# Kernel optimization log

Hardware: AMD Instinct MI355X
Metric: run time of the kernel (lower is better)

## Reference

```python
import jax, jax.numpy as jnp
import numpy as np

M = 16       # learned queries
K = 64       # top-k sparse tokens
HEADS = 4    # attention heads
LN_EPS = 1e-5


def _l2norm(x, eps=1e-12):
    n = jnp.linalg.norm(x, axis=-1, keepdims=True)
    return x / jnp.maximum(n, eps)


def _layernorm(x, w, b):
    mu = x.mean(-1, keepdims=True)
    var = x.var(-1, keepdims=True)
    return (x - mu) * jax.lax.rsqrt(var + LN_EPS) * w + b


def setup_inputs() -> dict:
    key = jax.random.key(0)
    ks = jax.random.split(key, 12)
    B, N, C, T, TD, D = 4, 16384, 1024, 20, 512, 64
    s = lambda k, sh: jax.random.normal(k, sh, jnp.float32) * 0.02
    return {
        "image_features": jax.random.normal(ks[0], (B, N, C), jnp.float32),
        "text_features": jax.random.normal(ks[1], (B, T, TD), jnp.float32),
        "Wd": s(ks[2], (C, D)), "bd": jnp.zeros((D,), jnp.float32),
        "Wu": s(ks[3], (D, C)), "bu": jnp.zeros((C,), jnp.float32),
        "m_queries": jax.random.normal(ks[4], (1, M, D), jnp.float32),
        "Wq": s(ks[5], (D, D)), "bq": jnp.zeros((D,), jnp.float32),
        "Wk": s(ks[6], (D, D)), "bk": jnp.zeros((D,), jnp.float32),
        "Wv": s(ks[7], (D, D)), "bv": jnp.zeros((D,), jnp.float32),
        "Wo": s(ks[8], (D, D)), "bo": jnp.zeros((D,), jnp.float32),
        "ln_w": jnp.ones((D,), jnp.float32), "ln_b": jnp.zeros((D,), jnp.float32),
        "gamma": jnp.float32(0.1),
    }


def reference(image_features, text_features, Wd, bd, Wu, bu, m_queries,
              Wq, bq, Wk, bk, Wv, bv, Wo, bo, ln_w, ln_b, gamma):
    B, N, C = image_features.shape
    D = Wd.shape[1]
    identity = image_features

    # down-project + exact GELU (dropout is identity at eval)
    a = jax.nn.gelu(image_features @ Wd + bd, approximate=False)  # [B,N,D]

    # tokens_of_interest=None, text_consistency_loss=False:
    # slice text to projected dim, take token 0 as key
    sel = text_features[:, 0, :D]                                  # [B,D]
    scores = jnp.einsum("bnd,bd->bn", _l2norm(a), _l2norm(sel))    # [B,N]

    # top-k mask -> nonzero gives row-sorted indices per batch
    _, idx = jax.lax.top_k(scores, K)                              # [B,K]
    idx = jnp.sort(idx, axis=1)

    sparse = jnp.take_along_axis(a, idx[:, :, None], axis=1)       # [B,K,D]
    queries = jnp.broadcast_to(m_queries, (B, M, D))
    comb = jnp.concatenate([queries, sparse], axis=1)              # [B,M+K,D]

    x = _layernorm(comb, ln_w, ln_b)
    H, Dh = HEADS, D // HEADS
    S = M + K
    q = (x @ Wq + bq).reshape(B, S, H, Dh)
    k = (x @ Wk + bk).reshape(B, S, H, Dh)
    v = (x @ Wv + bv).reshape(B, S, H, Dh)
    att = jnp.einsum("bshd,bthd->bhst", q, k) / jnp.sqrt(jnp.float32(Dh))
    att = jax.nn.softmax(att, axis=-1)
    o = jnp.einsum("bhst,bthd->bshd", att, v).reshape(B, S, D)
    attn_out = o @ Wo + bo

    enh = comb + attn_out
    enh_sparse = enh[:, M:, :]                                     # [B,K,D]

    # scatter enhanced sparse tokens back into full sequence
    brow = jnp.arange(B)[:, None]
    delta_proj = jnp.zeros_like(a).at[brow, idx].set(enh_sparse)   # [B,N,D]
    delta_x = delta_proj @ Wu + bu                                 # [B,N,C]

    return identity + delta_x * gamma
```

## Files before the change

kernel.cpp:

```cpp
#include <hip/hip_runtime.h>
#include <hip/hip_bf16.h>
#include <math.h>

typedef __bf16 bf16x8 __attribute__((ext_vector_type(8)));
typedef unsigned short u16x8 __attribute__((ext_vector_type(8)));
typedef float f32x4 __attribute__((ext_vector_type(4)));

#define CDIM 1024
#define DDIM 64
#define NB   16384
#define NROWS 65536

__device__ __forceinline__ unsigned short f2bf(float x){
  unsigned int u = __float_as_uint(x);
  unsigned int lsb = (u >> 16) & 1u;
  u += 0x7fffu + lsb;
  return (unsigned short)(u >> 16);
}

__global__ __launch_bounds__(256) void dsa_prep(
    const float* __restrict__ Wd, const float* __restrict__ tf,
    unsigned short* __restrict__ Wf, float* __restrict__ seln){
  int bb = blockIdx.x, tid = threadIdx.x;
  if (bb < 32){
    int g = bb*256 + tid;
    int lane = g & 63, tj = g >> 6;
    int n  = ((tj & 3) << 4) + (lane & 15);
    int k0 = ((tj >> 2) << 5) + ((lane >> 4) << 3);
    u16x8 uv;
    #pragma unroll
    for (int e=0;e<8;e++) uv[e] = f2bf(Wd[(k0+e)*DDIM + n]);
    *(u16x8*)(Wf + (size_t)g*8) = uv;
  } else {
    int w = tid >> 6, lane = tid & 63;
    float x = tf[w*(20*512) + lane];
    float sq = x*x;
    #pragma unroll
    for (int m=1; m<64; m<<=1) sq += __shfl_xor(sq, m);
    seln[w*64 + lane] = x / fmaxf(sqrtf(sq), 1e-12f);
  }
}

__global__ __launch_bounds__(256) void dsa_main(
    const float* __restrict__ X, const unsigned short* __restrict__ Wf,
    const float* __restrict__ bd, const float* __restrict__ bu,
    const float* __restrict__ gam, const float* __restrict__ seln,
    float* __restrict__ out, float* __restrict__ a_out, float* __restrict__ scores)
{
  const int tid  = threadIdx.x;
  const int lane = tid & 63, w = tid >> 6;
  const int row0 = blockIdx.x*64 + w*16;
  const int batch = blockIdx.x >> 8;
  const float gamma = gam[0];
  const int lr = lane & 15, lq = lane >> 4;

  const size_t rowoff = (size_t)(row0 + lr)*CDIM + lq*8;
  const float* xp = X   + rowoff;
  float*       op = out + rowoff;
  const float* bup = bu + lq*8;
  const bf16x8* wf8 = (const bf16x8*)Wf;

  f32x4 acc[4] = {};

  #pragma unroll 2
  for (int t = 0; t < 32; ++t){
    f32x4 xa = *(const f32x4*)(xp + t*32);
    f32x4 xb = *(const f32x4*)(xp + t*32 + 4);
    bf16x8 bv0 = wf8[(t*4+0)*64 + lane];
    bf16x8 bv1 = wf8[(t*4+1)*64 + lane];
    bf16x8 bv2 = wf8[(t*4+2)*64 + lane];
    bf16x8 bv3 = wf8[(t*4+3)*64 + lane];
    f32x4 ba = *(const f32x4*)(bup + t*32);
    f32x4 bb = *(const f32x4*)(bup + t*32 + 4);
    f32x4 oa = xa + gamma*ba;
    f32x4 ob = xb + gamma*bb;
    __builtin_nontemporal_store(oa, (f32x4*)(op + t*32));
    __builtin_nontemporal_store(ob, (f32x4*)(op + t*32 + 4));
    union { u16x8 u; bf16x8 b; } cv;
    cv.u[0]=f2bf(xa[0]); cv.u[1]=f2bf(xa[1]); cv.u[2]=f2bf(xa[2]); cv.u[3]=f2bf(xa[3]);
    cv.u[4]=f2bf(xb[0]); cv.u[5]=f2bf(xb[1]); cv.u[6]=f2bf(xb[2]); cv.u[7]=f2bf(xb[3]);
    acc[0] = __builtin_amdgcn_mfma_f32_16x16x32_bf16(cv.b, bv0, acc[0], 0,0,0);
    acc[1] = __builtin_amdgcn_mfma_f32_16x16x32_bf16(cv.b, bv1, acc[1], 0,0,0);
    acc[2] = __builtin_amdgcn_mfma_f32_16x16x32_bf16(cv.b, bv2, acc[2], 0,0,0);
    acc[3] = __builtin_amdgcn_mfma_f32_16x16x32_bf16(cv.b, bv3, acc[3], 0,0,0);
  }

  const float* selb = seln + batch*64;
  float ss[4] = {0,0,0,0}, dt[4] = {0,0,0,0};
  float gv[4][4];
  #pragma unroll
  for (int j=0;j<4;j++){
    int col = 16*j + lr;
    float bdc = bd[col];
    float sc  = selb[col];
    #pragma unroll
    for (int r=0;r<4;r++){
      float y = acc[j][r] + bdc;
      float g = 0.5f * y * (1.0f + erff(y * 0.70710678118654752f));
      gv[j][r] = g;
      ss[r] += g*g;
      dt[r] += g*sc;
    }
  }
  #pragma unroll
  for (int r=0;r<4;r++){
    int row = row0 + 4*lq + r;
    #pragma unroll
    for (int j=0;j<4;j++)
      a_out[(size_t)row*DDIM + 16*j + lr] = gv[j][r];
  }
  #pragma unroll
  for (int m=1;m<16;m<<=1){
    #pragma unroll
    for (int r=0;r<4;r++){
      ss[r] += __shfl_xor(ss[r], m);
      dt[r] += __shfl_xor(dt[r], m);
    }
  }
  if (lr == 0){
    #pragma unroll
    for (int r=0;r<4;r++)
      scores[row0 + 4*lq + r] = dt[r] / fmaxf(sqrtf(ss[r]), 1e-12f);
  }
}

__global__ __launch_bounds__(1024) void dsa_topk(const float* __restrict__ scores,
                                                 int* __restrict__ idxo){
  const int b = blockIdx.x, tid = threadIdx.x;
  const float* s = scores + b*NB;
  const int base = tid*16;
  unsigned key[16];
  #pragma unroll
  for (int i=0;i<16;i+=4){
    f32x4 f = *(const f32x4*)(s + base + i);
    #pragma unroll
    for (int c=0;c<4;c++){
      unsigned u = __float_as_uint(f[c]);
      key[i+c] = (u & 0x80000000u) ? ~u : (u | 0x80000000u);
    }
  }

  __shared__ unsigned bins[256];
  __shared__ unsigned sh_pref, sh_R;
  __shared__ int selIdx[64];
  __shared__ int eqIdx[256];
  __shared__ unsigned selCnt, eqCnt;

  unsigned prefix = 0, R = 64;
  for (int pass=0; pass<4; ++pass){
    const int shift = 24 - pass*8;
    if (tid < 256) bins[tid] = 0;
    __syncthreads();
    #pragma unroll
    for (int i=0;i<16;i++){
      unsigned k = key[i];
      bool ok;
      if (pass == 0) ok = true;
      else           ok = ((k >> (shift+8)) == prefix);
      if (ok) atomicAdd(&bins[(k >> shift) & 255u], 1u);
    }
    __syncthreads();
    if (tid < 64){
      unsigned c0 = bins[tid*4+0], c1 = bins[tid*4+1];
      unsigned c2 = bins[tid*4+2], c3 = bins[tid*4+3];
      unsigned gs = c0+c1+c2+c3;
      unsigned suf = gs;
      #pragma unroll
      for (int m=1;m<64;m<<=1){
        unsigned o = __shfl_down(suf, m);
        if (tid + m < 64) suf += o;
      }
      unsigned above = suf - gs;
      if (above < R && R <= suf){
        unsigned a3 = above;
        unsigned a2 = a3 + c3;
        unsigned a1 = a2 + c2;
        unsigned a0 = a1 + c1;
        unsigned bb, ab;
        if      (R <= a3 + c3){ bb = 3; ab = a3; }
        else if (R <= a2 + c2){ bb = 2; ab = a2; }
        else if (R <= a1 + c1){ bb = 1; ab = a1; }
        else                  { bb = 0; ab = a0; }
        sh_pref = (prefix << 8) | (tid*4 + bb);
        sh_R = R - ab;
      }
    }
    __syncthreads();
    prefix = sh_pref; R = sh_R;
    __syncthreads();
  }
  if (tid == 0){ selCnt = 0; eqCnt = 0; }
  __syncthreads();
  #pragma unroll
  for (int i=0;i<16;i++){
    unsigned k = key[i];
    if (k > prefix){
      selIdx[atomicAdd(&selCnt, 1u)] = base + i;
    } else if (k == prefix){
      unsigned p = atomicAdd(&eqCnt, 1u);
      if (p < 256) eqIdx[p] = base + i;
    }
  }
  __syncthreads();
  if (tid == 0){
    unsigned n = eqCnt < 256u ? eqCnt : 256u;
    unsigned have = selCnt;
    for (unsigned r2 = 0; r2 < R; ++r2){
      int best = 0x7fffffff, bi = -1;
      for (unsigned e=0; e<n; e++)
        if (eqIdx[e] < best){ best = eqIdx[e]; bi = (int)e; }
      selIdx[have + r2] = best;
      eqIdx[bi] = 0x7fffffff;
    }
  }
  __syncthreads();
  if (tid < 64){
    int x = selIdx[tid];
    #pragma unroll
    for (int size=2; size<=64; size<<=1){
      #pragma unroll
      for (int stride=size>>1; stride>0; stride>>=1){
        int ox = __shfl_xor(x, stride);
        bool up = ((tid & size) == 0);
        bool takeMin = (((tid & stride) == 0) == up);
        int mn = x < ox ? x : ox, mx = x < ox ? ox : x;
        x = takeMin ? mn : mx;
      }
    }
    idxo[b*64 + tid] = x;
  }
}

__global__ __launch_bounds__(512) void dsa_tail(
    const float* __restrict__ a, const float* __restrict__ mq, const int* __restrict__ idx,
    const float* __restrict__ lnw, const float* __restrict__ lnb,
    const float* __restrict__ Wq, const float* __restrict__ bq,
    const float* __restrict__ Wk, const float* __restrict__ bk,
    const float* __restrict__ Wv, const float* __restrict__ bv,
    const float* __restrict__ Wo, const float* __restrict__ bo,
    float* __restrict__ enh)
{
  __shared__ float xln[80][64];
  __shared__ float qS[80][64];
  __shared__ float vS[80][68];
  __shared__ float kT[64][81];
  __shared__ float oS[80][64];
  __shared__ float WoS[64][64];
  __shared__ float rowbuf[8][84];
  __shared__ int   sidx[64];

  const int b = blockIdx.x, tid = threadIdx.x;
  const int w = tid >> 6, lane = tid & 63;

  if (tid < 64) sidx[tid] = idx[b*64 + tid];
  for (int e = tid; e < 4096; e += 512) WoS[e>>6][e&63] = Wo[e];
  __syncthreads();

  {
    float lw = lnw[lane], lb = lnb[lane];
    float vals[10];
    #pragma unroll
    for (int i=0;i<10;i++){
      int s = w + 8*i;
      vals[i] = (s < 16) ? mq[s*64 + lane]
                         : a[((size_t)b*NB + sidx[s-16])*64 + lane];
    }
    #pragma unroll
    for (int i=0;i<10;i++){
      int s = w + 8*i;
      float val = vals[i];
      float sm = val, sq = val*val;
      #pragma unroll
      for (int m=1;m<64;m<<=1){ sm += __shfl_xor(sm,m); sq += __shfl_xor(sq,m); }
      float mu  = sm * (1.0f/64.0f);
      float var = sq * (1.0f/64.0f) - mu*mu;
      xln[s][lane] = (val - mu) * rsqrtf(var + 1e-5f) * lw + lb;
    }
  }
  __syncthreads();

  #pragma unroll 1
  for (int m = 0; m < 3; ++m){
    const float* Wm = (m==0) ? Wq : (m==1) ? Wk : Wv;
    const float* bm = (m==0) ? bq : (m==1) ? bk : bv;
    float wreg[64];
    #pragma unroll
    for (int c=0;c<64;c++) wreg[c] = Wm[c*64 + lane];
    float bias = bm[lane];
    #pragma unroll 1
    for (int s = w; s < 80; s += 8){
      float accv = bias;
      #pragma unroll
      for (int c4=0;c4<16;c4++){
        f32x4 x4 = *(const f32x4*)&xln[s][c4*4];
        accv += x4[0]*wreg[c4*4+0] + x4[1]*wreg[c4*4+1]
              + x4[2]*wreg[c4*4+2] + x4[3]*wreg[c4*4+3];
      }
      if (m==0)      qS[s][lane]  = accv;
      else if (m==1) kT[lane][s]  = accv;
      else           vS[s][lane]  = accv;
    }
  }
  __syncthreads();

  {
    const int h = w >> 1, h16 = h*16;
    const int i0 = 16 + (w & 1)*32;
    const int jj = lane >> 4, dd = lane & 15;
    #pragma unroll 2
    for (int ii = 0; ii < 32; ++ii){
      int i = i0 + ii;
      float v0 = 0.f, v1 = 0.f;
      #pragma unroll
      for (int d=0; d<16; ++d){
        float qd = qS[i][h16+d];
        v0 = fmaf(qd, kT[h16+d][lane],    v0);
        v1 = fmaf(qd, kT[h16+d][64 + dd], v1);
      }
      v0 *= 0.25f; v1 *= 0.25f;
      float mx = fmaxf(v0, v1);
      #pragma unroll
      for (int m2=1;m2<64;m2<<=1) mx = fmaxf(mx, __shfl_xor(mx,m2));
      float e0 = expf(v0 - mx);
      float e1 = expf(v1 - mx);
      float sm = e0 + ((lane < 16) ? e1 : 0.f);
      #pragma unroll
      for (int m2=1;m2<64;m2<<=1) sm += __shfl_xor(sm,m2);
      float inv = 1.0f / sm;
      rowbuf[w][lane] = e0 * inv;
      if (lane < 16) rowbuf[w][64+dd] = e1 * inv;
      float part = 0.f;
      #pragma unroll
      for (int tt=0; tt<20; ++tt){
        int j = jj*20 + tt;
        part = fmaf(rowbuf[w][j], vS[j][h16+dd], part);
      }
      part += __shfl_xor(part, 16);
      part += __shfl_xor(part, 32);
      if (lane < 16) oS[i][h16+dd] = part;
    }
  }
  __syncthreads();

  for (int e = tid; e < 4096; e += 512){
    int s16 = e >> 6, cc = e & 63;
    float accv = bo[cc];
    #pragma unroll
    for (int d4=0; d4<16; ++d4){
      f32x4 o4 = *(const f32x4*)&oS[16+s16][d4*4];
      accv += o4[0]*WoS[d4*4+0][cc] + o4[1]*WoS[d4*4+1][cc]
            + o4[2]*WoS[d4*4+2][cc] + o4[3]*WoS[d4*4+3][cc];
    }
    float cmb = a[((size_t)b*NB + sidx[s16])*64 + cc];
    enh[(b*64 + s16)*64 + cc] = cmb + accv;
  }
}

__global__ __launch_bounds__(256) void dsa_scatter(
    const float* __restrict__ enh, const float* __restrict__ Wu,
    const float* __restrict__ gam, const int* __restrict__ idx,
    float* __restrict__ out)
{
  int blk = blockIdx.x;
  int b = blk >> 6, j = blk & 63;
  int tid = threadIdx.x;
  __shared__ float er[64];
  if (tid < 64) er[tid] = enh[(b*64+j)*64 + tid];
  __syncthreads();
  int n = idx[b*64 + j];
  float gamma = gam[0];
  int c0 = tid*4;
  float ax=0.f, ay=0.f, az=0.f, aw=0.f;
  #pragma unroll 8
  for (int d=0; d<64; ++d){
    float ev = er[d];
    f32x4 wr = *(const f32x4*)(Wu + d*CDIM + c0);
    ax += ev*wr[0]; ay += ev*wr[1]; az += ev*wr[2]; aw += ev*wr[3];
  }
  float* op = out + ((size_t)b*NB + n)*CDIM + c0;
  f32x4 cu = *(f32x4*)op;
  cu[0] += gamma*ax; cu[1] += gamma*ay; cu[2] += gamma*az; cu[3] += gamma*aw;
  *(f32x4*)op = cu;
}

extern "C" void kernel_launch(void* const* d_in, const int* in_sizes, int n_in,
                              void* d_out, int out_size, void* d_ws, size_t ws_size,
                              hipStream_t stream) {
  const float* X    = (const float*)d_in[0];
  const float* tf   = (const float*)d_in[1];
  const float* Wd   = (const float*)d_in[2];
  const float* bd   = (const float*)d_in[3];
  const float* Wu   = (const float*)d_in[4];
  const float* bu   = (const float*)d_in[5];
  const float* mq   = (const float*)d_in[6];
  const float* Wq   = (const float*)d_in[7];
  const float* bq   = (const float*)d_in[8];
  const float* Wk   = (const float*)d_in[9];
  const float* bk   = (const float*)d_in[10];
  const float* Wv   = (const float*)d_in[11];
  const float* bv   = (const float*)d_in[12];
  const float* Wo   = (const float*)d_in[13];
  const float* bo   = (const float*)d_in[14];
  const float* lnw  = (const float*)d_in[15];
  const float* lnb  = (const float*)d_in[16];
  const float* gam  = (const float*)d_in[17];
  float* out = (float*)d_out;

  float* ws_a               = (float*)d_ws;
  unsigned short* ws_wf     = (unsigned short*)(ws_a + (size_t)NROWS*DDIM);
  float* ws_scores          = (float*)(ws_wf + 64*CDIM);
  float* ws_seln            = ws_scores + NROWS;
  int*   ws_idx             = (int*)(ws_seln + 256);
  float* ws_enh             = (float*)(ws_idx + 256);

  dsa_prep   <<<33,   256, 0, stream>>>(Wd, tf, ws_wf, ws_seln);
  dsa_main   <<<1024, 256, 0, stream>>>(X, ws_wf, bd, bu, gam, ws_seln,
                                        out, ws_a, ws_scores);
  dsa_topk   <<<4,   1024, 0, stream>>>(ws_scores, ws_idx);
  dsa_tail   <<<4,    512, 0, stream>>>(ws_a, mq, ws_idx, lnw, lnb,
                                        Wq, bq, Wk, bk, Wv, bv, Wo, bo, ws_enh);
  dsa_scatter<<<256,  256, 0, stream>>>(ws_enh, Wu, gam, ws_idx, out);
}
```

Baseline: 229.2 us.

## Stage Wd tiles in double-buffered LDS and software-pipeline X loads in main GEMM

The main down-projection kernel now copies the bf16 weight panel into a double-buffered shared-memory tile once per block instead of having every wave read it from global memory. It also prefetches the next chunk of X rows into registers while computing the current one. The gamma*bu bias is precomputed in the prep kernel and kept in LDS. Other changes: hardware bf16 conversion replaces the manual rounding, and the output stores are no longer nontemporal. The costs are more register pressure and LDS use (about 36 KB per block), plus block-wide syncs that may lower occupancy on this memory-bound streaming kernel.

```diff
diff --git a/kernel.cpp b/kernel.cpp
--- a/kernel.cpp
+++ b/kernel.cpp
@@ -20,7 +20,9 @@
 
 __global__ __launch_bounds__(256) void dsa_prep(
     const float* __restrict__ Wd, const float* __restrict__ tf,
-    unsigned short* __restrict__ Wf, float* __restrict__ seln){
+    const float* __restrict__ bu, const float* __restrict__ gam,
+    unsigned short* __restrict__ Wf, float* __restrict__ seln,
+    float* __restrict__ gbu){
   int bb = blockIdx.x, tid = threadIdx.x;
   if (bb < 32){
     int g = bb*256 + tid;
@@ -38,52 +40,91 @@
     #pragma unroll
     for (int m=1; m<64; m<<=1) sq += __shfl_xor(sq, m);
     seln[w*64 + lane] = x / fmaxf(sqrtf(sq), 1e-12f);
+    float g = gam[0];
+    f32x4 b4 = *(const f32x4*)(bu + tid*4);
+    *(f32x4*)(gbu + tid*4) = g*b4;
   }
 }
 
 __global__ __launch_bounds__(256) void dsa_main(
     const float* __restrict__ X, const unsigned short* __restrict__ Wf,
-    const float* __restrict__ bd, const float* __restrict__ bu,
-    const float* __restrict__ gam, const float* __restrict__ seln,
+    const float* __restrict__ bd, const float* __restrict__ gbu,
+    const float* __restrict__ seln,
     float* __restrict__ out, float* __restrict__ a_out, float* __restrict__ scores)
 {
+  __shared__ __align__(16) unsigned short Bs[2][8192];
+  __shared__ __align__(16) float gbS[1024];
   const int tid  = threadIdx.x;
   const int lane = tid & 63, w = tid >> 6;
+  const int lr = lane & 15, lq = lane >> 4;
   const int row0 = blockIdx.x*64 + w*16;
   const int batch = blockIdx.x >> 8;
-  const float gamma = gam[0];
-  const int lr = lane & 15, lq = lane >> 4;
 
   const size_t rowoff = (size_t)(row0 + lr)*CDIM + lq*8;
   const float* xp = X   + rowoff;
   float*       op = out + rowoff;
-  const float* bup = bu + lq*8;
-  const bf16x8* wf8 = (const bf16x8*)Wf;
-
+
+  f32x4 xr0[4][2], xr1[4][2];
+  uint4 st[4];
   f32x4 acc[4] = {};
 
-  #pragma unroll 2
-  for (int t = 0; t < 32; ++t){
-    f32x4 xa = *(const f32x4*)(xp + t*32);
-    f32x4 xb = *(const f32x4*)(xp + t*32 + 4);
-    bf16x8 bv0 = wf8[(t*4+0)*64 + lane];
-    bf16x8 bv1 = wf8[(t*4+1)*64 + lane];
-    bf16x8 bv2 = wf8[(t*4+2)*64 + lane];
-    bf16x8 bv3 = wf8[(t*4+3)*64 + lane];
-    f32x4 ba = *(const f32x4*)(bup + t*32);
-    f32x4 bb = *(const f32x4*)(bup + t*32 + 4);
-    f32x4 oa = xa + gamma*ba;
-    f32x4 ob = xb + gamma*bb;
-    __builtin_nontemporal_store(oa, (f32x4*)(op + t*32));
-    __builtin_nontemporal_store(ob, (f32x4*)(op + t*32 + 4));
-    union { u16x8 u; bf16x8 b; } cv;
-    cv.u[0]=f2bf(xa[0]); cv.u[1]=f2bf(xa[1]); cv.u[2]=f2bf(xa[2]); cv.u[3]=f2bf(xa[3]);
-    cv.u[4]=f2bf(xb[0]); cv.u[5]=f2bf(xb[1]); cv.u[6]=f2bf(xb[2]); cv.u[7]=f2bf(xb[3]);
-    acc[0] = __builtin_amdgcn_mfma_f32_16x16x32_bf16(cv.b, bv0, acc[0], 0,0,0);
-    acc[1] = __builtin_amdgcn_mfma_f32_16x16x32_bf16(cv.b, bv1, acc[1], 0,0,0);
-    acc[2] = __builtin_amdgcn_mfma_f32_16x16x32_bf16(cv.b, bv2, acc[2], 0,0,0);
-    acc[3] = __builtin_amdgcn_mfma_f32_16x16x32_bf16(cv.b, bv3, acc[3], 0,0,0);
-  }
+#define LD_B(P) { \
+    st[0] = *(const uint4*)(Wf + (P)*8192 + 0*2048 + tid*8); \
+    st[1] = *(const uint4*)(Wf + (P)*8192 + 1*2048 + tid*8); \
+    st[2] = *(const uint4*)(Wf + (P)*8192 + 2*2048 + tid*8); \
+    st[3] = *(const uint4*)(Wf + (P)*8192 + 3*2048 + tid*8); }
+#define ST_B(BUFI) { \
+    *(uint4*)(&Bs[BUFI][0*2048 + tid*8]) = st[0]; \
+    *(uint4*)(&Bs[BUFI][1*2048 + tid*8]) = st[1]; \
+    *(uint4*)(&Bs[BUFI][2*2048 + tid*8]) = st[2]; \
+    *(uint4*)(&Bs[BUFI][3*2048 + tid*8]) = st[3]; }
+#define LD_A(R, P) { \
+    R[0][0]=*(const f32x4*)(xp+(P)*128+  0); R[0][1]=*(const f32x4*)(xp+(P)*128+  4); \
+    R[1][0]=*(const f32x4*)(xp+(P)*128+ 32); R[1][1]=*(const f32x4*)(xp+(P)*128+ 36); \
+    R[2][0]=*(const f32x4*)(xp+(P)*128+ 64); R[2][1]=*(const f32x4*)(xp+(P)*128+ 68); \
+    R[3][0]=*(const f32x4*)(xp+(P)*128+ 96); R[3][1]=*(const f32x4*)(xp+(P)*128+100); }
+#define STEP(BUFI, TL, R, P) { \
+    f32x4 xa = R[TL][0], xb = R[TL][1]; \
+    f32x4 g0 = *(const f32x4*)(&gbS[(P)*128 + (TL)*32 + lq*8]); \
+    f32x4 g1 = *(const f32x4*)(&gbS[(P)*128 + (TL)*32 + lq*8 + 4]); \
+    *(f32x4*)(op + (P)*128 + (TL)*32)     = xa + g0; \
+    *(f32x4*)(op + (P)*128 + (TL)*32 + 4) = xb + g1; \
+    bf16x8 av; \
+    av[0]=(__bf16)xa[0]; av[1]=(__bf16)xa[1]; av[2]=(__bf16)xa[2]; av[3]=(__bf16)xa[3]; \
+    av[4]=(__bf16)xb[0]; av[5]=(__bf16)xb[1]; av[6]=(__bf16)xb[2]; av[7]=(__bf16)xb[3]; \
+    bf16x8 b0 = *(const bf16x8*)(&Bs[BUFI][(TL)*2048 + 0*512 + lane*8]); \
+    bf16x8 b1 = *(const bf16x8*)(&Bs[BUFI][(TL)*2048 + 1*512 + lane*8]); \
+    bf16x8 b2 = *(const bf16x8*)(&Bs[BUFI][(TL)*2048 + 2*512 + lane*8]); \
+    bf16x8 b3 = *(const bf16x8*)(&Bs[BUFI][(TL)*2048 + 3*512 + lane*8]); \
+    acc[0] = __builtin_amdgcn_mfma_f32_16x16x32_bf16(av, b0, acc[0], 0,0,0); \
+    acc[1] = __builtin_amdgcn_mfma_f32_16x16x32_bf16(av, b1, acc[1], 0,0,0); \
+    acc[2] = __builtin_amdgcn_mfma_f32_16x16x32_bf16(av, b2, acc[2], 0,0,0); \
+    acc[3] = __builtin_amdgcn_mfma_f32_16x16x32_bf16(av, b3, acc[3], 0,0,0); }
+#define PHASE(K, RCUR, RNXT) { \
+    LD_B((K)+1); LD_A(RNXT, (K)+1); \
+    STEP((K)&1, 0, RCUR, K) STEP((K)&1, 1, RCUR, K) \
+    STEP((K)&1, 2, RCUR, K) STEP((K)&1, 3, RCUR, K) \
+    ST_B(((K)+1)&1); __syncthreads(); }
+
+  { f32x4 t = *(const f32x4*)(gbu + tid*4); *(f32x4*)(&gbS[tid*4]) = t; }
+  LD_B(0); LD_A(xr0, 0);
+  ST_B(0);
+  __syncthreads();
+
+  PHASE(0, xr0, xr1)
+  PHASE(1, xr1, xr0)
+  PHASE(2, xr0, xr1)
+  PHASE(3, xr1, xr0)
+  PHASE(4, xr0, xr1)
+  PHASE(5, xr1, xr0)
+  PHASE(6, xr0, xr1)
+  STEP(1, 0, xr1, 7) STEP(1, 1, xr1, 7) STEP(1, 2, xr1, 7) STEP(1, 3, xr1, 7)
+
+#undef LD_B
+#undef ST_B
+#undef LD_A
+#undef STEP
+#undef PHASE
 
   const float* selb = seln + batch*64;
   float ss[4] = {0,0,0,0}, dt[4] = {0,0,0,0};
@@ -410,11 +451,12 @@
   unsigned short* ws_wf     = (unsigned short*)(ws_a + (size_t)NROWS*DDIM);
   float* ws_scores          = (float*)(ws_wf + 64*CDIM);
   float* ws_seln            = ws_scores + NROWS;
-  int*   ws_idx             = (int*)(ws_seln + 256);
+  float* ws_gbu             = ws_seln + 256;
+  int*   ws_idx             = (int*)(ws_gbu + 1024);
   float* ws_enh             = (float*)(ws_idx + 256);
 
-  dsa_prep   <<<33,   256, 0, stream>>>(Wd, tf, ws_wf, ws_seln);
-  dsa_main   <<<1024, 256, 0, stream>>>(X, ws_wf, bd, bu, gam, ws_seln,
+  dsa_prep   <<<33,   256, 0, stream>>>(Wd, tf, bu, gam, ws_wf, ws_seln, ws_gbu);
+  dsa_main   <<<1024, 256, 0, stream>>>(X, ws_wf, bd, ws_gbu, ws_seln,
                                         out, ws_a, ws_scores);
   dsa_topk   <<<4,   1024, 0, stream>>>(ws_scores, ws_idx);
   dsa_tail   <<<4,    512, 0, stream>>>(ws_a, mq, ws_idx, lnw, lnb,
```

After: 211.7 us. -7.6%, faster.

## Double-buffer X tiles into LDS via async global_load_lds in main GEMM

Applied to the files above, without the earlier changes.

The main down-projection kernel now streams each wave's 16x1024 slice of X into a swizzled, double-buffered LDS region using direct global-to-LDS loads. This overlaps the next chunk's fetch with the current chunk's MFMA and output writes. gamma*bu is precomputed once in the prep kernel and staged in LDS, and the output stores become ordinary stores instead of nontemporal ones. The bf16 conversion now uses a native cast rather than manual rounding. The manual vmcnt waits make correctness depend on counting outstanding loads exactly, and the 36KB of LDS per block limits occupancy.

```diff
diff --git a/kernel.cpp b/kernel.cpp
--- a/kernel.cpp
+++ b/kernel.cpp
@@ -18,9 +18,17 @@
   return (unsigned short)(u >> 16);
 }
 
+__device__ __forceinline__ void load_lds16(const float* g, float* l){
+  __builtin_amdgcn_global_load_lds(
+      (const __attribute__((address_space(1))) void*)g,
+      (__attribute__((address_space(3))) void*)l, 16, 0, 0);
+}
+
 __global__ __launch_bounds__(256) void dsa_prep(
     const float* __restrict__ Wd, const float* __restrict__ tf,
-    unsigned short* __restrict__ Wf, float* __restrict__ seln){
+    const float* __restrict__ bu, const float* __restrict__ gam,
+    unsigned short* __restrict__ Wf, float* __restrict__ seln,
+    float* __restrict__ gbu){
   int bb = blockIdx.x, tid = threadIdx.x;
   if (bb < 32){
     int g = bb*256 + tid;
@@ -38,52 +46,94 @@
     #pragma unroll
     for (int m=1; m<64; m<<=1) sq += __shfl_xor(sq, m);
     seln[w*64 + lane] = x / fmaxf(sqrtf(sq), 1e-12f);
-  }
-}
-
-__global__ __launch_bounds__(256) void dsa_main(
+    float g = gam[0];
+    f32x4 b4 = *(const f32x4*)(bu + tid*4);
+    *(f32x4*)(gbu + tid*4) = g*b4;
+  }
+}
+
+__global__ __launch_bounds__(256, 4) void dsa_main(
     const float* __restrict__ X, const unsigned short* __restrict__ Wf,
-    const float* __restrict__ bd, const float* __restrict__ bu,
-    const float* __restrict__ gam, const float* __restrict__ seln,
+    const float* __restrict__ bd, const float* __restrict__ gbu,
+    const float* __restrict__ seln,
     float* __restrict__ out, float* __restrict__ a_out, float* __restrict__ scores)
 {
+  __shared__ __align__(16) float AsF[8192];
+  __shared__ __align__(16) float gbS[1024];
   const int tid  = threadIdx.x;
   const int lane = tid & 63, w = tid >> 6;
+  const int lr = lane & 15, lq = lane >> 4;
   const int row0 = blockIdx.x*64 + w*16;
   const int batch = blockIdx.x >> 8;
-  const float gamma = gam[0];
-  const int lr = lane & 15, lq = lane >> 4;
-
-  const size_t rowoff = (size_t)(row0 + lr)*CDIM + lq*8;
-  const float* xp = X   + rowoff;
-  float*       op = out + rowoff;
-  const float* bup = bu + lq*8;
+
+  { f32x4 t = *(const f32x4*)(gbu + tid*4); *(f32x4*)(gbS + tid*4) = t; }
+  __syncthreads();
+
+  const int rsub = lane >> 4;
+  const int ch   = lane & 15;
+  const float* gbase = X + (size_t)(row0 + rsub)*CDIM;
+  float* asw = AsF + w*2048;
+  float* op  = out + (size_t)(row0 + lr)*CDIM;
   const bf16x8* wf8 = (const bf16x8*)Wf;
 
+  bf16x8 B[8];
   f32x4 acc[4] = {};
 
-  #pragma unroll 2
-  for (int t = 0; t < 32; ++t){
-    f32x4 xa = *(const f32x4*)(xp + t*32);
-    f32x4 xb = *(const f32x4*)(xp + t*32 + 4);
-    bf16x8 bv0 = wf8[(t*4+0)*64 + lane];
-    bf16x8 bv1 = wf8[(t*4+1)*64 + lane];
-    bf16x8 bv2 = wf8[(t*4+2)*64 + lane];
-    bf16x8 bv3 = wf8[(t*4+3)*64 + lane];
-    f32x4 ba = *(const f32x4*)(bup + t*32);
-    f32x4 bb = *(const f32x4*)(bup + t*32 + 4);
-    f32x4 oa = xa + gamma*ba;
-    f32x4 ob = xb + gamma*bb;
-    __builtin_nontemporal_store(oa, (f32x4*)(op + t*32));
-    __builtin_nontemporal_store(ob, (f32x4*)(op + t*32 + 4));
-    union { u16x8 u; bf16x8 b; } cv;
-    cv.u[0]=f2bf(xa[0]); cv.u[1]=f2bf(xa[1]); cv.u[2]=f2bf(xa[2]); cv.u[3]=f2bf(xa[3]);
-    cv.u[4]=f2bf(xb[0]); cv.u[5]=f2bf(xb[1]); cv.u[6]=f2bf(xb[2]); cv.u[7]=f2bf(xb[3]);
-    acc[0] = __builtin_amdgcn_mfma_f32_16x16x32_bf16(cv.b, bv0, acc[0], 0,0,0);
-    acc[1] = __builtin_amdgcn_mfma_f32_16x16x32_bf16(cv.b, bv1, acc[1], 0,0,0);
-    acc[2] = __builtin_amdgcn_mfma_f32_16x16x32_bf16(cv.b, bv2, acc[2], 0,0,0);
-    acc[3] = __builtin_amdgcn_mfma_f32_16x16x32_bf16(cv.b, bv3, acc[3], 0,0,0);
-  }
+#define DMA(P, SL) { \
+    { int gc = ch ^ ((0*4 + rsub)&7); \
+      load_lds16(gbase + (size_t)(0*4)*CDIM + (P)*64 + gc*4, asw + (SL)*1024 + 0*256); } \
+    { int gc = ch ^ ((1*4 + rsub)&7); \
+      load_lds16(gbase + (size_t)(1*4)*CDIM + (P)*64 + gc*4, asw + (SL)*1024 + 1*256); } \
+    { int gc = ch ^ ((2*4 + rsub)&7); \
+      load_lds16(gbase + (size_t)(2*4)*CDIM + (P)*64 + gc*4, asw + (SL)*1024 + 2*256); } \
+    { int gc = ch ^ ((3*4 + rsub)&7); \
+      load_lds16(gbase + (size_t)(3*4)*CDIM + (P)*64 + gc*4, asw + (SL)*1024 + 3*256); } }
+
+#define LDB(P) { \
+    B[0] = wf8[(((P)*2+0)*4+0)*64 + lane]; \
+    B[1] = wf8[(((P)*2+0)*4+1)*64 + lane]; \
+    B[2] = wf8[(((P)*2+0)*4+2)*64 + lane]; \
+    B[3] = wf8[(((P)*2+0)*4+3)*64 + lane]; \
+    B[4] = wf8[(((P)*2+1)*4+0)*64 + lane]; \
+    B[5] = wf8[(((P)*2+1)*4+1)*64 + lane]; \
+    B[6] = wf8[(((P)*2+1)*4+2)*64 + lane]; \
+    B[7] = wf8[(((P)*2+1)*4+3)*64 + lane]; }
+
+#define STEP(P, S, SL) { \
+    int c0 = (((S)*8 + lq*2 + 0) ^ (lr & 7)); \
+    int c1 = (((S)*8 + lq*2 + 1) ^ (lr & 7)); \
+    f32x4 xa = *(const f32x4*)(asw + (SL)*1024 + lr*64 + c0*4); \
+    f32x4 xb = *(const f32x4*)(asw + (SL)*1024 + lr*64 + c1*4); \
+    f32x4 g0 = *(const f32x4*)(gbS + (P)*64 + (S)*32 + lq*8); \
+    f32x4 g1 = *(const f32x4*)(gbS + (P)*64 + (S)*32 + lq*8 + 4); \
+    *(f32x4*)(op + (P)*64 + (S)*32 + lq*8)     = xa + g0; \
+    *(f32x4*)(op + (P)*64 + (S)*32 + lq*8 + 4) = xb + g1; \
+    bf16x8 av; \
+    av[0]=(__bf16)xa[0]; av[1]=(__bf16)xa[1]; av[2]=(__bf16)xa[2]; av[3]=(__bf16)xa[3]; \
+    av[4]=(__bf16)xb[0]; av[5]=(__bf16)xb[1]; av[6]=(__bf16)xb[2]; av[7]=(__bf16)xb[3]; \
+    acc[0] = __builtin_amdgcn_mfma_f32_16x16x32_bf16(av, B[4*(S)+0], acc[0], 0,0,0); \
+    acc[1] = __builtin_amdgcn_mfma_f32_16x16x32_bf16(av, B[4*(S)+1], acc[1], 0,0,0); \
+    acc[2] = __builtin_amdgcn_mfma_f32_16x16x32_bf16(av, B[4*(S)+2], acc[2], 0,0,0); \
+    acc[3] = __builtin_amdgcn_mfma_f32_16x16x32_bf16(av, B[4*(S)+3], acc[3], 0,0,0); }
+
+#define PH(P) { \
+    DMA((P)+1, ((P)+1)&1) \
+    LDB(P) \
+    asm volatile("s_waitcnt vmcnt(12)" ::: "memory"); \
+    STEP(P, 0, (P)&1) STEP(P, 1, (P)&1) \
+    asm volatile("" ::: "memory"); }
+
+  DMA(0, 0)
+  PH(0)  PH(1)  PH(2)  PH(3)  PH(4)  PH(5)  PH(6)  PH(7)
+  PH(8)  PH(9)  PH(10) PH(11) PH(12) PH(13) PH(14)
+  LDB(15)
+  asm volatile("s_waitcnt vmcnt(8)" ::: "memory");
+  STEP(15, 0, 1) STEP(15, 1, 1)
+
+#undef DMA
+#undef LDB
+#undef STEP
+#undef PH
 
   const float* selb = seln + batch*64;
   float ss[4] = {0,0,0,0}, dt[4] = {0,0,0,0};
@@ -410,11 +460,12 @@
   unsigned short* ws_wf     = (unsigned short*)(ws_a + (size_t)NROWS*DDIM);
   float* ws_scores          = (float*)(ws_wf + 64*CDIM);
   float* ws_seln            = ws_scores + NROWS;
-  int*   ws_idx             = (int*)(ws_seln + 256);
+  float* ws_gbu             = ws_seln + 256;
+  int*   ws_idx             = (int*)(ws_gbu + 1024);
   float* ws_enh             = (float*)(ws_idx + 256);
 
-  dsa_prep   <<<33,   256, 0, stream>>>(Wd, tf, ws_wf, ws_seln);
-  dsa_main   <<<1024, 256, 0, stream>>>(X, ws_wf, bd, bu, gam, ws_seln,
+  dsa_prep   <<<33,   256, 0, stream>>>(Wd, tf, bu, gam, ws_wf, ws_seln, ws_gbu);
+  dsa_main   <<<1024, 256, 0, stream>>>(X, ws_wf, bd, ws_gbu, ws_seln,
                                         out, ws_a, ws_scores);
   dsa_topk   <<<4,   1024, 0, stream>>>(ws_scores, ws_idx);
   dsa_tail   <<<4,    512, 0, stream>>>(ws_a, mq, ws_idx, lnw, lnb,
```

Result: faster. 220.8 us (-3.7%).

## Software-pipeline X and weight loads in main GEMM loop and precompute gamma*bu

Applied to the files above, without the earlier changes.

The main streaming loop now prefetches X tiles and bf16 weight fragments two iterations ahead using a triple-buffered register ring, and the loop is fully unrolled. gamma*bu is precomputed in the prep kernel and staged into shared memory, so the loop no longer reads bu from global memory or multiplies by gamma. Output stores become regular stores instead of nontemporal stores, and the float-to-bf16 conversion switches from a manual rounding routine to the native cast. The aim is to hide global memory latency in a bandwidth-bound loop, at the cost of more register pressure, which may reduce occupancy.

```diff
diff --git a/kernel.cpp b/kernel.cpp
--- a/kernel.cpp
+++ b/kernel.cpp
@@ -20,7 +20,9 @@
 
 __global__ __launch_bounds__(256) void dsa_prep(
     const float* __restrict__ Wd, const float* __restrict__ tf,
-    unsigned short* __restrict__ Wf, float* __restrict__ seln){
+    const float* __restrict__ bu, const float* __restrict__ gam,
+    unsigned short* __restrict__ Wf, float* __restrict__ seln,
+    float* __restrict__ gbu){
   int bb = blockIdx.x, tid = threadIdx.x;
   if (bb < 32){
     int g = bb*256 + tid;
@@ -38,52 +40,63 @@
     #pragma unroll
     for (int m=1; m<64; m<<=1) sq += __shfl_xor(sq, m);
     seln[w*64 + lane] = x / fmaxf(sqrtf(sq), 1e-12f);
+    float g = gam[0];
+    f32x4 b4 = *(const f32x4*)(bu + tid*4);
+    *(f32x4*)(gbu + tid*4) = g*b4;
   }
 }
 
 __global__ __launch_bounds__(256) void dsa_main(
     const float* __restrict__ X, const unsigned short* __restrict__ Wf,
-    const float* __restrict__ bd, const float* __restrict__ bu,
-    const float* __restrict__ gam, const float* __restrict__ seln,
+    const float* __restrict__ bd, const float* __restrict__ gbu,
+    const float* __restrict__ seln,
     float* __restrict__ out, float* __restrict__ a_out, float* __restrict__ scores)
 {
+  __shared__ __align__(16) float gbS[1024];
   const int tid  = threadIdx.x;
   const int lane = tid & 63, w = tid >> 6;
+  const int lr = lane & 15, lq = lane >> 4;
   const int row0 = blockIdx.x*64 + w*16;
   const int batch = blockIdx.x >> 8;
-  const float gamma = gam[0];
-  const int lr = lane & 15, lq = lane >> 4;
-
-  const size_t rowoff = (size_t)(row0 + lr)*CDIM + lq*8;
-  const float* xp = X   + rowoff;
-  float*       op = out + rowoff;
-  const float* bup = bu + lq*8;
+
+  { f32x4 t = *(const f32x4*)(gbu + tid*4); *(f32x4*)(gbS + tid*4) = t; }
+  __syncthreads();
+
+  const float* xp = X   + (size_t)(row0 + lr)*CDIM + lq*8;
+  float*       op = out + (size_t)(row0 + lr)*CDIM + lq*8;
   const bf16x8* wf8 = (const bf16x8*)Wf;
 
-  f32x4 acc[4] = {};
-
-  #pragma unroll 2
+  f32x4  xa[3], xb[3];
+  bf16x8 B[3][4];
+  f32x4  acc[4] = {};
+
+#define LDX(T) { xa[(T)%3] = *(const f32x4*)(xp + (T)*32); \
+                 xb[(T)%3] = *(const f32x4*)(xp + (T)*32 + 4); }
+#define LDBF(T) { B[(T)%3][0] = wf8[((T)*4+0)*64 + lane]; \
+                  B[(T)%3][1] = wf8[((T)*4+1)*64 + lane]; \
+                  B[(T)%3][2] = wf8[((T)*4+2)*64 + lane]; \
+                  B[(T)%3][3] = wf8[((T)*4+3)*64 + lane]; }
+
+  LDX(0) LDBF(0)
+  LDX(1) LDBF(1)
+  #pragma unroll
   for (int t = 0; t < 32; ++t){
-    f32x4 xa = *(const f32x4*)(xp + t*32);
-    f32x4 xb = *(const f32x4*)(xp + t*32 + 4);
-    bf16x8 bv0 = wf8[(t*4+0)*64 + lane];
-    bf16x8 bv1 = wf8[(t*4+1)*64 + lane];
-    bf16x8 bv2 = wf8[(t*4+2)*64 + lane];
-    bf16x8 bv3 = wf8[(t*4+3)*64 + lane];
-    f32x4 ba = *(const f32x4*)(bup + t*32);
-    f32x4 bb = *(const f32x4*)(bup + t*32 + 4);
-    f32x4 oa = xa + gamma*ba;
-    f32x4 ob = xb + gamma*bb;
-    __builtin_nontemporal_store(oa, (f32x4*)(op + t*32));
-    __builtin_nontemporal_store(ob, (f32x4*)(op + t*32 + 4));
-    union { u16x8 u; bf16x8 b; } cv;
-    cv.u[0]=f2bf(xa[0]); cv.u[1]=f2bf(xa[1]); cv.u[2]=f2bf(xa[2]); cv.u[3]=f2bf(xa[3]);
-    cv.u[4]=f2bf(xb[0]); cv.u[5]=f2bf(xb[1]); cv.u[6]=f2bf(xb[2]); cv.u[7]=f2bf(xb[3]);
-    acc[0] = __builtin_amdgcn_mfma_f32_16x16x32_bf16(cv.b, bv0, acc[0], 0,0,0);
-    acc[1] = __builtin_amdgcn_mfma_f32_16x16x32_bf16(cv.b, bv1, acc[1], 0,0,0);
-    acc[2] = __builtin_amdgcn_mfma_f32_16x16x32_bf16(cv.b, bv2, acc[2], 0,0,0);
-    acc[3] = __builtin_amdgcn_mfma_f32_16x16x32_bf16(cv.b, bv3, acc[3], 0,0,0);
-  }
+    if (t + 2 < 32){ LDX(t+2) LDBF(t+2) }
+    f32x4 g0 = *(const f32x4*)(gbS + t*32 + lq*8);
+    f32x4 g1 = *(const f32x4*)(gbS + t*32 + lq*8 + 4);
+    f32x4 va = xa[t%3], vb = xb[t%3];
+    *(f32x4*)(op + t*32)     = va + g0;
+    *(f32x4*)(op + t*32 + 4) = vb + g1;
+    bf16x8 av;
+    av[0]=(__bf16)va[0]; av[1]=(__bf16)va[1]; av[2]=(__bf16)va[2]; av[3]=(__bf16)va[3];
+    av[4]=(__bf16)vb[0]; av[5]=(__bf16)vb[1]; av[6]=(__bf16)vb[2]; av[7]=(__bf16)vb[3];
+    acc[0] = __builtin_amdgcn_mfma_f32_16x16x32_bf16(av, B[t%3][0], acc[0], 0,0,0);
+    acc[1] = __builtin_amdgcn_mfma_f32_16x16x32_bf16(av, B[t%3][1], acc[1], 0,0,0);
+    acc[2] = __builtin_amdgcn_mfma_f32_16x16x32_bf16(av, B[t%3][2], acc[2], 0,0,0);
+    acc[3] = __builtin_amdgcn_mfma_f32_16x16x32_bf16(av, B[t%3][3], acc[3], 0,0,0);
+  }
+#undef LDX
+#undef LDBF
 
   const float* selb = seln + batch*64;
   float ss[4] = {0,0,0,0}, dt[4] = {0,0,0,0};
@@ -410,11 +423,12 @@
   unsigned short* ws_wf     = (unsigned short*)(ws_a + (size_t)NROWS*DDIM);
   float* ws_scores          = (float*)(ws_wf + 64*CDIM);
   float* ws_seln            = ws_scores + NROWS;
-  int*   ws_idx             = (int*)(ws_seln + 256);
+  float* ws_gbu             = ws_seln + 256;
+  int*   ws_idx             = (int*)(ws_gbu + 1024);
   float* ws_enh             = (float*)(ws_idx + 256);
 
-  dsa_prep   <<<33,   256, 0, stream>>>(Wd, tf, ws_wf, ws_seln);
-  dsa_main   <<<1024, 256, 0, stream>>>(X, ws_wf, bd, bu, gam, ws_seln,
+  dsa_prep   <<<33,   256, 0, stream>>>(Wd, tf, bu, gam, ws_wf, ws_seln, ws_gbu);
+  dsa_main   <<<1024, 256, 0, stream>>>(X, ws_wf, bd, ws_gbu, ws_seln,
                                         out, ws_a, ws_scores);
   dsa_topk   <<<4,   1024, 0, stream>>>(ws_scores, ws_idx);
   dsa_tail   <<<4,    512, 0, stream>>>(ws_a, mq, ws_idx, lnw, lnb,
```

Result: slower. 240.8 us (+5.0%).
